# Optimization experiments

Measured on AMD Instinct MI355X. Metric: run time of the kernel, lower is better.

## Reference

```python
import jax, jax.numpy as jnp
import numpy as np
from jax import lax

DIM = 192
K = 3
K2 = K * K


def _conv1x1(x, W, b):
    # x: [B,C,H,W], W: [O,C], b: [O]
    return jnp.einsum('oc,bchw->bohw', W, x) + b[None, :, None, None]


def setup_inputs() -> dict:
    key = jax.random.key(0)
    ks = jax.random.split(key, 10)
    B, C, H, Wd = 16, DIM, 96, 96
    s = 1.0 / np.sqrt(C)
    x = jax.random.normal(ks[0], (B, C, H, Wd), dtype=jnp.float32)
    Wk = jax.random.uniform(ks[1], (C, C), jnp.float32, -s, s)
    bk = jax.random.uniform(ks[2], (C,), jnp.float32, -s, s)
    sg = 1.0 / np.sqrt(K2)
    Wg = jax.random.uniform(ks[3], (K2, K2), jnp.float32, -sg, sg)
    bg = jax.random.uniform(ks[4], (K2,), jnp.float32, -sg, sg)
    Wx = jax.random.uniform(ks[5], (C, C), jnp.float32, -s, s)
    bx = jax.random.uniform(ks[6], (C,), jnp.float32, -s, s)
    Wp = jax.random.uniform(ks[7], (C, C), jnp.float32, -s, s)
    bp = jax.random.uniform(ks[8], (C,), jnp.float32, -s, s)
    dc = jnp.zeros((C,), jnp.float32)  # difference_control init
    return {"x": x, "Wk": Wk, "bk": bk, "Wg": Wg, "bg": bg,
            "Wx": Wx, "bx": bx, "Wp": Wp, "bp": bp, "dc": dc}


def reference(x, Wk, bk, Wg, bg, Wx, bx, Wp, bp, dc):
    B, C, H, Wd = x.shape
    L = H * Wd
    # --- kernel generation ---
    k = _conv1x1(x, Wk, bk)                       # [B,C,H,W]
    k = k.reshape(B, C, K2, L // K2).mean(-1)     # AdaptiveAvgPool1d(9), L % 9 == 0
    k = jax.nn.gelu(k, approximate=False)         # torch nn.GELU (exact erf)
    k = k @ Wg.T + bg                             # Linear(9,9)
    k = k.reshape(B, C, K, K)
    # --- kernel mean difference ---
    mean_k = k.mean(axis=(2, 3), keepdims=True)
    factor = jax.nn.sigmoid(dc)[None, :, None, None]
    k = k - factor * mean_k
    # --- dynamic depthwise conv, groups = B*C ---
    xp = _conv1x1(x, Wx, bx)
    lhs = xp.reshape(1, B * C, H, Wd)
    rhs = k.reshape(B * C, 1, K, K)
    y = lax.conv_general_dilated(
        lhs, rhs, window_strides=(1, 1), padding='SAME',
        dimension_numbers=('NCHW', 'OIHW', 'NCHW'),
        feature_group_count=B * C)
    y = y.reshape(B, C, H, Wd)
    return _conv1x1(y, Wp, bp)
```

## Files before the change

kernel.cpp:

```cpp
#include <hip/hip_runtime.h>
#include <math.h>

#define CDIM 192
#define HWP 9216
#define WIMG 96
#define HIMG 96
#define BDIM 16

typedef float f32x4 __attribute__((ext_vector_type(4)));
typedef short bf16x8 __attribute__((ext_vector_type(8)));

__device__ __forceinline__ ushort f2bf(float f) {
    uint u = __builtin_bit_cast(uint, f);
    u += 0x7FFFu + ((u >> 16) & 1);
    return (ushort)(u >> 16);
}
__device__ __forceinline__ float bf2f(ushort h) {
    return __builtin_bit_cast(float, (uint)h << 16);
}

__global__ void prep_wfrag_kernel(const float* __restrict__ Wx, const float* __restrict__ Wp,
                                  ushort* __restrict__ WxF, ushort* __restrict__ WpF) {
    int t = blockIdx.x * 256 + threadIdx.x;
    int m = t / 4608;
    int r = t % 4608;
    int ks = r / 768, nf = (r / 64) % 12, l = r % 64;
    const float* W = m ? Wp : Wx;
    ushort* F = m ? WpF : WxF;
    int o = nf * 16 + (l & 15);
    int c0 = ks * 32 + (l >> 4) * 8;
    float4 a = *(const float4*)&W[o * CDIM + c0];
    float4 b = *(const float4*)&W[o * CDIM + c0 + 4];
    ushort* dst = F + (size_t)r * 8;
    dst[0] = f2bf(a.x); dst[1] = f2bf(a.y); dst[2] = f2bf(a.z); dst[3] = f2bf(a.w);
    dst[4] = f2bf(b.x); dst[5] = f2bf(b.y); dst[6] = f2bf(b.z); dst[7] = f2bf(b.w);
}

template<int IN_BF16, int OUT_BF16, int DO_POOL>
__global__ __launch_bounds__(256, 2) void convmfma_kernel(
    const void* __restrict__ in_, const ushort* __restrict__ Wf,
    const float* __restrict__ bias, void* __restrict__ out_,
    float* __restrict__ px) {
    const int p0 = blockIdx.x * 64;
    const int b = blockIdx.y;
    const int tid = threadIdx.x;
    const int l = tid & 63, w = tid >> 6;
    const size_t inplane = (size_t)CDIM * HWP;

    __shared__ __align__(16) ushort S[64 * 200];

#pragma unroll
    for (int it = 0; it < 3; ++it) {
        int u = tid + it * 256;
        int p4 = (u & 15) * 4, c4 = (u >> 4) * 4;
        ushort vv[4][4];
        if (IN_BF16) {
            const ushort* inb = (const ushort*)in_ + (size_t)b * inplane;
#pragma unroll
            for (int r = 0; r < 4; ++r) {
                ushort4 t4 = *(const ushort4*)(inb + (size_t)(c4 + r) * HWP + p0 + p4);
                vv[r][0] = t4.x; vv[r][1] = t4.y; vv[r][2] = t4.z; vv[r][3] = t4.w;
            }
        } else {
            const float* inb = (const float*)in_ + (size_t)b * inplane;
#pragma unroll
            for (int r = 0; r < 4; ++r) {
                float4 t4 = *(const float4*)(inb + (size_t)(c4 + r) * HWP + p0 + p4);
                vv[r][0] = f2bf(t4.x); vv[r][1] = f2bf(t4.y);
                vv[r][2] = f2bf(t4.z); vv[r][3] = f2bf(t4.w);
            }
        }
#pragma unroll
        for (int q = 0; q < 4; ++q) {
            *(ushort4*)&S[(p4 + q) * 200 + c4] =
                make_ushort4(vv[0][q], vv[1][q], vv[2][q], vv[3][q]);
        }
    }
    __syncthreads();

    if (DO_POOL) {
        if (tid < CDIM) {
            float s = 0.f;
#pragma unroll 8
            for (int p = 0; p < 64; ++p) s += bf2f(S[p * 200 + tid]);
            atomicAdd(&px[(b * CDIM + tid) * 9 + (p0 >> 10)], s);
        }
    }

    f32x4 acc[12];
#pragma unroll
    for (int nf = 0; nf < 12; ++nf) {
        float bv = bias[nf * 16 + (l & 15)];
        acc[nf] = (f32x4){bv, bv, bv, bv};
    }

    const ushort* Sp = &S[(w * 16 + (l & 15)) * 200];
    const int g8 = (l >> 4) * 8;
#pragma unroll
    for (int ks = 0; ks < 6; ++ks) {
        bf16x8 a = *(const bf16x8*)(Sp + ks * 32 + g8);
#pragma unroll
        for (int nf = 0; nf < 12; ++nf) {
            bf16x8 bb = *(const bf16x8*)&Wf[(size_t)((ks * 12 + nf) * 64 + l) * 8];
            acc[nf] = __builtin_amdgcn_mfma_f32_16x16x32_bf16(a, bb, acc[nf], 0, 0, 0);
        }
    }

    const int p_out = p0 + w * 16 + (l >> 4) * 4;
#pragma unroll
    for (int nf = 0; nf < 12; ++nf) {
        int o = nf * 16 + (l & 15);
        if (OUT_BF16) {
            ushort* ob = (ushort*)out_ + (size_t)b * inplane + (size_t)o * HWP + p_out;
            *(ushort4*)ob = make_ushort4(f2bf(acc[nf][0]), f2bf(acc[nf][1]),
                                         f2bf(acc[nf][2]), f2bf(acc[nf][3]));
        } else {
            float* ob = (float*)out_ + (size_t)b * inplane + (size_t)o * HWP + p_out;
            *(float4*)ob = make_float4(acc[nf][0], acc[nf][1], acc[nf][2], acc[nf][3]);
        }
    }
}

__global__ void make_kernels_kernel(const float* __restrict__ px,
                                    const float* __restrict__ Wk, const float* __restrict__ bk,
                                    const float* __restrict__ Wg, const float* __restrict__ bg,
                                    const float* __restrict__ dc,
                                    float* __restrict__ kk) {
    int b = blockIdx.x;
    int o = threadIdx.x;
    __shared__ float pxs[CDIM * 9];
    for (int i = threadIdx.x; i < CDIM * 9; i += blockDim.x)
        pxs[i] = px[b * CDIM * 9 + i] * (1.0f / 1024.0f);
    __syncthreads();
    float k1[9];
    float bias = bk[o];
#pragma unroll
    for (int j = 0; j < 9; j++) k1[j] = bias;
    for (int c = 0; c < CDIM; c++) {
        float w = Wk[o * CDIM + c];
#pragma unroll
        for (int j = 0; j < 9; j++) k1[j] = fmaf(w, pxs[c * 9 + j], k1[j]);
    }
#pragma unroll
    for (int j = 0; j < 9; j++) {
        float v = k1[j];
        k1[j] = 0.5f * v * (1.0f + erff(v * 0.70710678118654752f));
    }
    float k2[9];
    float mean = 0.f;
#pragma unroll
    for (int i = 0; i < 9; i++) {
        float a = bg[i];
#pragma unroll
        for (int j = 0; j < 9; j++) a = fmaf(k1[j], Wg[i * 9 + j], a);
        k2[i] = a;
        mean += a;
    }
    mean *= (1.0f / 9.0f);
    float f = 1.0f / (1.0f + expf(-dc[o]));
    float sub = f * mean;
#pragma unroll
    for (int i = 0; i < 9; i++) kk[(b * CDIM + o) * 9 + i] = k2[i] - sub;
}

#define SROW 100
template<int OUT_BF16>
__global__ __launch_bounds__(256) void dwconv_kernel_bf16(const ushort* __restrict__ xp,
                                                          const float* __restrict__ kk,
                                                          void* __restrict__ y_) {
    int bc = blockIdx.x >> 1;
    int row0 = (blockIdx.x & 1) * 48;
    int tid = threadIdx.x;

    __shared__ __align__(16) float Sbuf[4 + 50 * SROW + 4];
    float* S = Sbuf + 4;

    float kv[9];
#pragma unroll
    for (int j = 0; j < 9; j++) kv[j] = kk[bc * 9 + j];

    float4 z4 = make_float4(0.f, 0.f, 0.f, 0.f);
    for (int i = tid; i < (4 + 50 * SROW + 4) / 4; i += 256) ((float4*)Sbuf)[i] = z4;
    __syncthreads();

    const ushort* src = xp + (size_t)bc * HWP;
    for (int i = tid; i < 50 * 24; i += 256) {
        int s = i / 24, j4 = i % 24;
        int hh = row0 - 1 + s;
        if (hh >= 0 && hh < HIMG) {
            ushort4 v = *(const ushort4*)(src + (size_t)hh * WIMG + 4 * j4);
            *(float4*)&S[s * SROW + 4 * j4] =
                make_float4(bf2f(v.x), bf2f(v.y), bf2f(v.z), bf2f(v.w));
        }
    }
    __syncthreads();

    for (int i = tid; i < 48 * 24; i += 256) {
        int h = i / 24, wg = i % 24;
        float a0 = 0.f, a1 = 0.f, a2 = 0.f, a3 = 0.f;
#pragma unroll
        for (int r = 0; r < 3; r++) {
            const float* row = &S[(h + r) * SROW + 4 * wg];
            float left = row[-1];
            float4 m = *(const float4*)row;
            float r4 = row[4];
            float c0 = kv[r * 3 + 0], c1 = kv[r * 3 + 1], c2 = kv[r * 3 + 2];
            a0 = fmaf(c0, left, fmaf(c1, m.x, fmaf(c2, m.y, a0)));
            a1 = fmaf(c0, m.x, fmaf(c1, m.y, fmaf(c2, m.z, a1)));
            a2 = fmaf(c0, m.y, fmaf(c1, m.z, fmaf(c2, m.w, a2)));
            a3 = fmaf(c0, m.z, fmaf(c1, m.w, fmaf(c2, r4, a3)));
        }
        if (OUT_BF16) {
            ushort* dst = (ushort*)y_ + (size_t)bc * HWP;
            *(ushort4*)(dst + (size_t)(row0 + h) * WIMG + 4 * wg) =
                make_ushort4(f2bf(a0), f2bf(a1), f2bf(a2), f2bf(a3));
        } else {
            float* dst = (float*)y_ + (size_t)bc * HWP;
            *(float4*)(dst + (size_t)(row0 + h) * WIMG + 4 * wg) =
                make_float4(a0, a1, a2, a3);
        }
    }
}

extern "C" void kernel_launch(void* const* d_in, const int* in_sizes, int n_in,
                              void* d_out, int out_size, void* d_ws, size_t ws_size,
                              hipStream_t stream) {
    const float* x  = (const float*)d_in[0];
    const float* Wk = (const float*)d_in[1];
    const float* bk = (const float*)d_in[2];
    const float* Wg = (const float*)d_in[3];
    const float* bg = (const float*)d_in[4];
    const float* Wx = (const float*)d_in[5];
    const float* bx = (const float*)d_in[6];
    const float* Wp = (const float*)d_in[7];
    const float* bp = (const float*)d_in[8];
    const float* dc = (const float*)d_in[9];
    float* out = (float*)d_out;

    char* ws = (char*)d_ws;
    size_t off_WxF = 0;
    size_t off_WpF = off_WxF + 36864 * 2;
    size_t off_px  = off_WpF + 36864 * 2;
    size_t off_kk  = off_px + 27648 * 4;
    size_t off_xp  = off_kk + 27648 * 4;
    size_t xp_bytes = (size_t)BDIM * CDIM * HWP * 2;
    size_t off_y   = off_xp + xp_bytes;

    ushort* WxF = (ushort*)(ws + off_WxF);
    ushort* WpF = (ushort*)(ws + off_WpF);
    float*  px  = (float*)(ws + off_px);
    float*  kkp = (float*)(ws + off_kk);
    ushort* xp  = (ushort*)(ws + off_xp);
    bool y_in_ws = (ws_size >= off_y + xp_bytes);

    hipMemsetAsync(px, 0, 27648 * 4, stream);
    prep_wfrag_kernel<<<dim3(36), dim3(256), 0, stream>>>(Wx, Wp, WxF, WpF);
    convmfma_kernel<0, 1, 1><<<dim3(HWP / 64, BDIM), dim3(256), 0, stream>>>(
        (const void*)x, WxF, bx, (void*)xp, px);
    make_kernels_kernel<<<dim3(BDIM), dim3(CDIM), 0, stream>>>(px, Wk, bk, Wg, bg, dc, kkp);

    if (y_in_ws) {
        ushort* y = (ushort*)(ws + off_y);
        dwconv_kernel_bf16<1><<<dim3(BDIM * CDIM * 2), dim3(256), 0, stream>>>(xp, kkp, (void*)y);
        convmfma_kernel<1, 0, 0><<<dim3(HWP / 64, BDIM), dim3(256), 0, stream>>>(
            (const void*)y, WpF, bp, (void*)out, nullptr);
    } else {
        dwconv_kernel_bf16<0><<<dim3(BDIM * CDIM * 2), dim3(256), 0, stream>>>(xp, kkp, (void*)out);
        convmfma_kernel<0, 0, 0><<<dim3(HWP / 64, BDIM), dim3(256), 0, stream>>>(
            (const void*)out, WpF, bp, (void*)out, nullptr);
    }
}
```

Before: 341.4 us.

## Load MFMA A-operands directly from global, drop LDS staging, raise occupancy

The 1x1-conv MFMA kernel no longer stages the input tile through shared memory. Each lane now loads its A fragments straight from global memory with scalar strided loads, and the pooling sum is done with wave shuffles plus atomics instead of an LDS column sum. Launch bounds go from 2 to 3 blocks per SM, and the make_kernels kernel now stages Wk through padded shared memory to avoid uncoalesced per-thread row reads. The direct loads are scalar 2- or 4-byte accesses strided by a full plane, which risks poorer coalescing, more memory instructions, and more atomics than the previous vectorized LDS transpose.

```diff
diff --git a/kernel.cpp b/kernel.cpp
--- a/kernel.cpp
+++ b/kernel.cpp
@@ -37,7 +37,7 @@
 }
 
 template<int IN_BF16, int OUT_BF16, int DO_POOL>
-__global__ __launch_bounds__(256, 2) void convmfma_kernel(
+__global__ __launch_bounds__(256, 3) void convmfma_kernel(
     const void* __restrict__ in_, const ushort* __restrict__ Wf,
     const float* __restrict__ bias, void* __restrict__ out_,
     float* __restrict__ px) {
@@ -45,46 +45,45 @@
     const int b = blockIdx.y;
     const int tid = threadIdx.x;
     const int l = tid & 63, w = tid >> 6;
-    const size_t inplane = (size_t)CDIM * HWP;
-
-    __shared__ __align__(16) ushort S[64 * 200];
-
-#pragma unroll
-    for (int it = 0; it < 3; ++it) {
-        int u = tid + it * 256;
-        int p4 = (u & 15) * 4, c4 = (u >> 4) * 4;
-        ushort vv[4][4];
-        if (IN_BF16) {
-            const ushort* inb = (const ushort*)in_ + (size_t)b * inplane;
-#pragma unroll
-            for (int r = 0; r < 4; ++r) {
-                ushort4 t4 = *(const ushort4*)(inb + (size_t)(c4 + r) * HWP + p0 + p4);
-                vv[r][0] = t4.x; vv[r][1] = t4.y; vv[r][2] = t4.z; vv[r][3] = t4.w;
-            }
-        } else {
-            const float* inb = (const float*)in_ + (size_t)b * inplane;
-#pragma unroll
-            for (int r = 0; r < 4; ++r) {
-                float4 t4 = *(const float4*)(inb + (size_t)(c4 + r) * HWP + p0 + p4);
-                vv[r][0] = f2bf(t4.x); vv[r][1] = f2bf(t4.y);
-                vv[r][2] = f2bf(t4.z); vv[r][3] = f2bf(t4.w);
-            }
-        }
-#pragma unroll
-        for (int q = 0; q < 4; ++q) {
-            *(ushort4*)&S[(p4 + q) * 200 + c4] =
-                make_ushort4(vv[0][q], vv[1][q], vv[2][q], vv[3][q]);
-        }
-    }
-    __syncthreads();
-
-    if (DO_POOL) {
-        if (tid < CDIM) {
-            float s = 0.f;
-#pragma unroll 8
-            for (int p = 0; p < 64; ++p) s += bf2f(S[p * 200 + tid]);
-            atomicAdd(&px[(b * CDIM + tid) * 9 + (p0 >> 10)], s);
-        }
+    const size_t plane = (size_t)CDIM * HWP;
+    const int pA = p0 + w * 16 + (l & 15);
+    const int g8 = (l >> 4) * 8;
+
+    bf16x8 a[6];
+    if (IN_BF16) {
+        const ushort* inb = (const ushort*)in_ + (size_t)b * plane + pA;
+#pragma unroll
+        for (int ks = 0; ks < 6; ++ks) {
+#pragma unroll
+            for (int i = 0; i < 8; ++i)
+                a[ks][i] = (short)inb[(size_t)(ks * 32 + g8 + i) * HWP];
+        }
+    } else {
+        const float* inb = (const float*)in_ + (size_t)b * plane + pA;
+        float af[6][8];
+#pragma unroll
+        for (int ks = 0; ks < 6; ++ks)
+#pragma unroll
+            for (int i = 0; i < 8; ++i)
+                af[ks][i] = inb[(size_t)(ks * 32 + g8 + i) * HWP];
+        if (DO_POOL) {
+#pragma unroll
+            for (int ks = 0; ks < 6; ++ks)
+#pragma unroll
+                for (int i = 0; i < 8; ++i) {
+                    float s = af[ks][i];
+                    s += __shfl_xor(s, 1, 64);
+                    s += __shfl_xor(s, 2, 64);
+                    s += __shfl_xor(s, 4, 64);
+                    s += __shfl_xor(s, 8, 64);
+                    if ((l & 15) == 0)
+                        atomicAdd(&px[(b * CDIM + ks * 32 + g8 + i) * 9 + (p0 >> 10)], s);
+                }
+        }
+#pragma unroll
+        for (int ks = 0; ks < 6; ++ks)
+#pragma unroll
+            for (int i = 0; i < 8; ++i) a[ks][i] = (short)f2bf(af[ks][i]);
     }
 
     f32x4 acc[12];
@@ -94,15 +93,12 @@
         acc[nf] = (f32x4){bv, bv, bv, bv};
     }
 
-    const ushort* Sp = &S[(w * 16 + (l & 15)) * 200];
-    const int g8 = (l >> 4) * 8;
 #pragma unroll
     for (int ks = 0; ks < 6; ++ks) {
-        bf16x8 a = *(const bf16x8*)(Sp + ks * 32 + g8);
 #pragma unroll
         for (int nf = 0; nf < 12; ++nf) {
             bf16x8 bb = *(const bf16x8*)&Wf[(size_t)((ks * 12 + nf) * 64 + l) * 8];
-            acc[nf] = __builtin_amdgcn_mfma_f32_16x16x32_bf16(a, bb, acc[nf], 0, 0, 0);
+            acc[nf] = __builtin_amdgcn_mfma_f32_16x16x32_bf16(a[ks], bb, acc[nf], 0, 0, 0);
         }
     }
 
@@ -111,11 +107,11 @@
     for (int nf = 0; nf < 12; ++nf) {
         int o = nf * 16 + (l & 15);
         if (OUT_BF16) {
-            ushort* ob = (ushort*)out_ + (size_t)b * inplane + (size_t)o * HWP + p_out;
+            ushort* ob = (ushort*)out_ + (size_t)b * plane + (size_t)o * HWP + p_out;
             *(ushort4*)ob = make_ushort4(f2bf(acc[nf][0]), f2bf(acc[nf][1]),
                                          f2bf(acc[nf][2]), f2bf(acc[nf][3]));
         } else {
-            float* ob = (float*)out_ + (size_t)b * inplane + (size_t)o * HWP + p_out;
+            float* ob = (float*)out_ + (size_t)b * plane + (size_t)o * HWP + p_out;
             *(float4*)ob = make_float4(acc[nf][0], acc[nf][1], acc[nf][2], acc[nf][3]);
         }
     }
@@ -129,17 +125,27 @@
     int b = blockIdx.x;
     int o = threadIdx.x;
     __shared__ float pxs[CDIM * 9];
-    for (int i = threadIdx.x; i < CDIM * 9; i += blockDim.x)
+    __shared__ float WkS[CDIM][33];
+    for (int i = threadIdx.x; i < CDIM * 9; i += CDIM)
         pxs[i] = px[b * CDIM * 9 + i] * (1.0f / 1024.0f);
-    __syncthreads();
     float k1[9];
     float bias = bk[o];
 #pragma unroll
     for (int j = 0; j < 9; j++) k1[j] = bias;
-    for (int c = 0; c < CDIM; c++) {
-        float w = Wk[o * CDIM + c];
-#pragma unroll
-        for (int j = 0; j < 9; j++) k1[j] = fmaf(w, pxs[c * 9 + j], k1[j]);
+
+    for (int c0 = 0; c0 < CDIM; c0 += 32) {
+        __syncthreads();
+        for (int i = threadIdx.x; i < CDIM * 32; i += CDIM) {
+            int oo = i >> 5, cc = i & 31;
+            WkS[oo][cc] = Wk[oo * CDIM + c0 + cc];
+        }
+        __syncthreads();
+#pragma unroll 4
+        for (int cc = 0; cc < 32; ++cc) {
+            float wv = WkS[o][cc];
+#pragma unroll
+            for (int j = 0; j < 9; j++) k1[j] = fmaf(wv, pxs[(c0 + cc) * 9 + j], k1[j]);
+        }
     }
 #pragma unroll
     for (int j = 0; j < 9; j++) {
```

Result: slower. 450.4 us (+31.9%).

## Switch intermediates to channels-last layout with swizzled LDS and direct MFMA loads

Applied to the files above, without the earlier changes.

The xp and y intermediates are now stored in channels-last (pixel-major) bf16 layout. The first 1x1 conv transposes its output through XOR-swizzled LDS so the writes are coalesced. The second 1x1 conv loads its A fragments straight from global memory with no LDS staging. The depthwise conv becomes one thread per 8 channels per pixel, reading neighbours as 16-byte vectors with transposed kernel weights, and make_kernels now tiles Wk through LDS. This removes the LDS transpose in conv2 and the separate plane staging in dwconv, at the cost of the dwconv reading neighbours from global or cache nine times.

```diff
diff --git a/kernel.cpp b/kernel.cpp
--- a/kernel.cpp
+++ b/kernel.cpp
@@ -17,6 +17,10 @@
 }
 __device__ __forceinline__ float bf2f(ushort h) {
     return __builtin_bit_cast(float, (uint)h << 16);
+}
+
+__device__ __forceinline__ int sidx(int p, int c) {
+    return (p << 8) + (c ^ ((((p >> 2) ^ p) & 7) << 3));
 }
 
 __global__ void prep_wfrag_kernel(const float* __restrict__ Wx, const float* __restrict__ Wp,
@@ -36,55 +40,41 @@
     dst[4] = f2bf(b.x); dst[5] = f2bf(b.y); dst[6] = f2bf(b.z); dst[7] = f2bf(b.w);
 }
 
-template<int IN_BF16, int OUT_BF16, int DO_POOL>
-__global__ __launch_bounds__(256, 2) void convmfma_kernel(
-    const void* __restrict__ in_, const ushort* __restrict__ Wf,
-    const float* __restrict__ bias, void* __restrict__ out_,
+__global__ __launch_bounds__(256, 2) void conv1_kernel(
+    const float* __restrict__ x, const ushort* __restrict__ Wf,
+    const float* __restrict__ bias, ushort* __restrict__ xp,
     float* __restrict__ px) {
     const int p0 = blockIdx.x * 64;
     const int b = blockIdx.y;
     const int tid = threadIdx.x;
     const int l = tid & 63, w = tid >> 6;
-    const size_t inplane = (size_t)CDIM * HWP;
-
-    __shared__ __align__(16) ushort S[64 * 200];
-
+
+    __shared__ __align__(16) ushort S[64 * 256];
+
+    const float* inb = x + (size_t)b * CDIM * HWP;
 #pragma unroll
     for (int it = 0; it < 3; ++it) {
         int u = tid + it * 256;
         int p4 = (u & 15) * 4, c4 = (u >> 4) * 4;
         ushort vv[4][4];
-        if (IN_BF16) {
-            const ushort* inb = (const ushort*)in_ + (size_t)b * inplane;
-#pragma unroll
-            for (int r = 0; r < 4; ++r) {
-                ushort4 t4 = *(const ushort4*)(inb + (size_t)(c4 + r) * HWP + p0 + p4);
-                vv[r][0] = t4.x; vv[r][1] = t4.y; vv[r][2] = t4.z; vv[r][3] = t4.w;
-            }
-        } else {
-            const float* inb = (const float*)in_ + (size_t)b * inplane;
-#pragma unroll
-            for (int r = 0; r < 4; ++r) {
-                float4 t4 = *(const float4*)(inb + (size_t)(c4 + r) * HWP + p0 + p4);
-                vv[r][0] = f2bf(t4.x); vv[r][1] = f2bf(t4.y);
-                vv[r][2] = f2bf(t4.z); vv[r][3] = f2bf(t4.w);
-            }
-        }
-#pragma unroll
-        for (int q = 0; q < 4; ++q) {
-            *(ushort4*)&S[(p4 + q) * 200 + c4] =
+#pragma unroll
+        for (int r = 0; r < 4; ++r) {
+            float4 t4 = *(const float4*)(inb + (size_t)(c4 + r) * HWP + p0 + p4);
+            vv[r][0] = f2bf(t4.x); vv[r][1] = f2bf(t4.y);
+            vv[r][2] = f2bf(t4.z); vv[r][3] = f2bf(t4.w);
+        }
+#pragma unroll
+        for (int q = 0; q < 4; ++q)
+            *(ushort4*)&S[sidx(p4 + q, c4)] =
                 make_ushort4(vv[0][q], vv[1][q], vv[2][q], vv[3][q]);
-        }
     }
     __syncthreads();
 
-    if (DO_POOL) {
-        if (tid < CDIM) {
-            float s = 0.f;
+    if (tid < CDIM) {
+        float s = 0.f;
 #pragma unroll 8
-            for (int p = 0; p < 64; ++p) s += bf2f(S[p * 200 + tid]);
-            atomicAdd(&px[(b * CDIM + tid) * 9 + (p0 >> 10)], s);
-        }
+        for (int p = 0; p < 64; ++p) s += bf2f(S[sidx(p, tid)]);
+        atomicAdd(&px[(b * CDIM + tid) * 9 + (p0 >> 10)], s);
     }
 
     f32x4 acc[12];
@@ -94,30 +84,73 @@
         acc[nf] = (f32x4){bv, bv, bv, bv};
     }
 
-    const ushort* Sp = &S[(w * 16 + (l & 15)) * 200];
     const int g8 = (l >> 4) * 8;
+    const int prow = w * 16 + (l & 15);
 #pragma unroll
     for (int ks = 0; ks < 6; ++ks) {
-        bf16x8 a = *(const bf16x8*)(Sp + ks * 32 + g8);
+        bf16x8 a = *(const bf16x8*)&S[sidx(prow, ks * 32 + g8)];
 #pragma unroll
         for (int nf = 0; nf < 12; ++nf) {
             bf16x8 bb = *(const bf16x8*)&Wf[(size_t)((ks * 12 + nf) * 64 + l) * 8];
             acc[nf] = __builtin_amdgcn_mfma_f32_16x16x32_bf16(a, bb, acc[nf], 0, 0, 0);
         }
     }
+    __syncthreads();
+
+    const int pw = w * 16 + (l >> 4) * 4;
+#pragma unroll
+    for (int nf = 0; nf < 12; ++nf) {
+        int o = nf * 16 + (l & 15);
+#pragma unroll
+        for (int q = 0; q < 4; ++q) S[sidx(pw + q, o)] = f2bf(acc[nf][q]);
+    }
+    __syncthreads();
+
+    ushort* ob = xp + ((size_t)b * HWP + p0) * CDIM;
+#pragma unroll
+    for (int it = 0; it < 6; ++it) {
+        int u = tid + it * 256;
+        int r = u / 24, cg = u % 24;
+        *(bf16x8*)(ob + (size_t)r * CDIM + cg * 8) = *(const bf16x8*)&S[sidx(r, cg * 8)];
+    }
+}
+
+__global__ __launch_bounds__(256, 3) void conv2_kernel(
+    const ushort* __restrict__ y, const ushort* __restrict__ Wf,
+    const float* __restrict__ bias, float* __restrict__ out) {
+    const int p0 = blockIdx.x * 64;
+    const int b = blockIdx.y;
+    const int l = threadIdx.x & 63, w = threadIdx.x >> 6;
+    const int g8 = (l >> 4) * 8;
+    const int pA = p0 + w * 16 + (l & 15);
+
+    const ushort* yb = y + ((size_t)b * HWP + pA) * CDIM + g8;
+    bf16x8 a[6];
+#pragma unroll
+    for (int ks = 0; ks < 6; ++ks) a[ks] = *(const bf16x8*)(yb + ks * 32);
+
+    f32x4 acc[12];
+#pragma unroll
+    for (int nf = 0; nf < 12; ++nf) {
+        float bv = bias[nf * 16 + (l & 15)];
+        acc[nf] = (f32x4){bv, bv, bv, bv};
+    }
+#pragma unroll
+    for (int ks = 0; ks < 6; ++ks) {
+#pragma unroll
+        for (int nf = 0; nf < 12; ++nf) {
+            bf16x8 bb = *(const bf16x8*)&Wf[(size_t)((ks * 12 + nf) * 64 + l) * 8];
+            acc[nf] = __builtin_amdgcn_mfma_f32_16x16x32_bf16(a[ks], bb, acc[nf], 0, 0, 0);
+        }
+    }
 
     const int p_out = p0 + w * 16 + (l >> 4) * 4;
+    float* ob = out + (size_t)b * CDIM * HWP + p_out;
 #pragma unroll
     for (int nf = 0; nf < 12; ++nf) {
         int o = nf * 16 + (l & 15);
-        if (OUT_BF16) {
-            ushort* ob = (ushort*)out_ + (size_t)b * inplane + (size_t)o * HWP + p_out;
-            *(ushort4*)ob = make_ushort4(f2bf(acc[nf][0]), f2bf(acc[nf][1]),
-                                         f2bf(acc[nf][2]), f2bf(acc[nf][3]));
-        } else {
-            float* ob = (float*)out_ + (size_t)b * inplane + (size_t)o * HWP + p_out;
-            *(float4*)ob = make_float4(acc[nf][0], acc[nf][1], acc[nf][2], acc[nf][3]);
-        }
+        *(float4*)(ob + (size_t)o * HWP) =
+            make_float4(acc[nf][0], acc[nf][1], acc[nf][2], acc[nf][3]);
     }
 }
 
@@ -125,21 +158,31 @@
                                     const float* __restrict__ Wk, const float* __restrict__ bk,
                                     const float* __restrict__ Wg, const float* __restrict__ bg,
                                     const float* __restrict__ dc,
-                                    float* __restrict__ kk) {
+                                    float* __restrict__ kkT) {
     int b = blockIdx.x;
     int o = threadIdx.x;
     __shared__ float pxs[CDIM * 9];
-    for (int i = threadIdx.x; i < CDIM * 9; i += blockDim.x)
+    __shared__ float WkS[CDIM][33];
+    for (int i = threadIdx.x; i < CDIM * 9; i += CDIM)
         pxs[i] = px[b * CDIM * 9 + i] * (1.0f / 1024.0f);
-    __syncthreads();
     float k1[9];
     float bias = bk[o];
 #pragma unroll
     for (int j = 0; j < 9; j++) k1[j] = bias;
-    for (int c = 0; c < CDIM; c++) {
-        float w = Wk[o * CDIM + c];
-#pragma unroll
-        for (int j = 0; j < 9; j++) k1[j] = fmaf(w, pxs[c * 9 + j], k1[j]);
+
+    for (int c0 = 0; c0 < CDIM; c0 += 32) {
+        __syncthreads();
+        for (int i = threadIdx.x; i < CDIM * 32; i += CDIM) {
+            int oo = i >> 5, cc = i & 31;
+            WkS[oo][cc] = Wk[oo * CDIM + c0 + cc];
+        }
+        __syncthreads();
+#pragma unroll 4
+        for (int cc = 0; cc < 32; ++cc) {
+            float wv = WkS[o][cc];
+#pragma unroll
+            for (int j = 0; j < 9; j++) k1[j] = fmaf(wv, pxs[(c0 + cc) * 9 + j], k1[j]);
+        }
     }
 #pragma unroll
     for (int j = 0; j < 9; j++) {
@@ -160,66 +203,52 @@
     float f = 1.0f / (1.0f + expf(-dc[o]));
     float sub = f * mean;
 #pragma unroll
-    for (int i = 0; i < 9; i++) kk[(b * CDIM + o) * 9 + i] = k2[i] - sub;
-}
-
-#define SROW 100
-template<int OUT_BF16>
-__global__ __launch_bounds__(256) void dwconv_kernel_bf16(const ushort* __restrict__ xp,
-                                                          const float* __restrict__ kk,
-                                                          void* __restrict__ y_) {
-    int bc = blockIdx.x >> 1;
-    int row0 = (blockIdx.x & 1) * 48;
-    int tid = threadIdx.x;
-
-    __shared__ __align__(16) float Sbuf[4 + 50 * SROW + 4];
-    float* S = Sbuf + 4;
-
-    float kv[9];
-#pragma unroll
-    for (int j = 0; j < 9; j++) kv[j] = kk[bc * 9 + j];
-
-    float4 z4 = make_float4(0.f, 0.f, 0.f, 0.f);
-    for (int i = tid; i < (4 + 50 * SROW + 4) / 4; i += 256) ((float4*)Sbuf)[i] = z4;
-    __syncthreads();
-
-    const ushort* src = xp + (size_t)bc * HWP;
-    for (int i = tid; i < 50 * 24; i += 256) {
-        int s = i / 24, j4 = i % 24;
-        int hh = row0 - 1 + s;
-        if (hh >= 0 && hh < HIMG) {
-            ushort4 v = *(const ushort4*)(src + (size_t)hh * WIMG + 4 * j4);
-            *(float4*)&S[s * SROW + 4 * j4] =
-                make_float4(bf2f(v.x), bf2f(v.y), bf2f(v.z), bf2f(v.w));
-        }
-    }
-    __syncthreads();
-
-    for (int i = tid; i < 48 * 24; i += 256) {
-        int h = i / 24, wg = i % 24;
-        float a0 = 0.f, a1 = 0.f, a2 = 0.f, a3 = 0.f;
-#pragma unroll
-        for (int r = 0; r < 3; r++) {
-            const float* row = &S[(h + r) * SROW + 4 * wg];
-            float left = row[-1];
-            float4 m = *(const float4*)row;
-            float r4 = row[4];
-            float c0 = kv[r * 3 + 0], c1 = kv[r * 3 + 1], c2 = kv[r * 3 + 2];
-            a0 = fmaf(c0, left, fmaf(c1, m.x, fmaf(c2, m.y, a0)));
-            a1 = fmaf(c0, m.x, fmaf(c1, m.y, fmaf(c2, m.z, a1)));
-            a2 = fmaf(c0, m.y, fmaf(c1, m.z, fmaf(c2, m.w, a2)));
-            a3 = fmaf(c0, m.z, fmaf(c1, m.w, fmaf(c2, r4, a3)));
-        }
-        if (OUT_BF16) {
-            ushort* dst = (ushort*)y_ + (size_t)bc * HWP;
-            *(ushort4*)(dst + (size_t)(row0 + h) * WIMG + 4 * wg) =
-                make_ushort4(f2bf(a0), f2bf(a1), f2bf(a2), f2bf(a3));
-        } else {
-            float* dst = (float*)y_ + (size_t)bc * HWP;
-            *(float4*)(dst + (size_t)(row0 + h) * WIMG + 4 * wg) =
-                make_float4(a0, a1, a2, a3);
-        }
-    }
+    for (int i = 0; i < 9; i++) kkT[(b * 9 + i) * CDIM + o] = k2[i] - sub;
+}
+
+__global__ __launch_bounds__(256) void dwconv_cl_kernel(const ushort* __restrict__ xp,
+                                                        const float* __restrict__ kkT,
+                                                        ushort* __restrict__ y) {
+    int idx = blockIdx.x * 256 + threadIdx.x;
+    int cg = idx % 24;
+    int pb = idx / 24;
+    int p = pb % HWP, b = pb / HWP;
+    int h = p / WIMG, wq = p % WIMG;
+
+    const ushort* base = xp + (size_t)pb * CDIM + cg * 8;
+    const float* kb = kkT + (size_t)b * 9 * CDIM + cg * 8;
+
+    float acc[8];
+#pragma unroll
+    for (int i = 0; i < 8; ++i) acc[i] = 0.f;
+
+#pragma unroll
+    for (int dh = -1; dh <= 1; ++dh) {
+        int hh = h + dh;
+        if (hh < 0 || hh >= HIMG) continue;
+#pragma unroll
+        for (int dw = -1; dw <= 1; ++dw) {
+            int ww = wq + dw;
+            if (ww < 0 || ww >= WIMG) continue;
+            int j = (dh + 1) * 3 + (dw + 1);
+            bf16x8 v = *(const bf16x8*)(base + (ptrdiff_t)(dh * WIMG + dw) * CDIM);
+            float4 k0 = *(const float4*)(kb + j * CDIM);
+            float4 k1 = *(const float4*)(kb + j * CDIM + 4);
+            acc[0] = fmaf(bf2f((ushort)v[0]), k0.x, acc[0]);
+            acc[1] = fmaf(bf2f((ushort)v[1]), k0.y, acc[1]);
+            acc[2] = fmaf(bf2f((ushort)v[2]), k0.z, acc[2]);
+            acc[3] = fmaf(bf2f((ushort)v[3]), k0.w, acc[3]);
+            acc[4] = fmaf(bf2f((ushort)v[4]), k1.x, acc[4]);
+            acc[5] = fmaf(bf2f((ushort)v[5]), k1.y, acc[5]);
+            acc[6] = fmaf(bf2f((ushort)v[6]), k1.z, acc[6]);
+            acc[7] = fmaf(bf2f((ushort)v[7]), k1.w, acc[7]);
+        }
+    }
+    ushort* dst = y + (size_t)pb * CDIM + cg * 8;
+    ushort4 o0 = make_ushort4(f2bf(acc[0]), f2bf(acc[1]), f2bf(acc[2]), f2bf(acc[3]));
+    ushort4 o1 = make_ushort4(f2bf(acc[4]), f2bf(acc[5]), f2bf(acc[6]), f2bf(acc[7]));
+    *(ushort4*)dst = o0;
+    *(ushort4*)(dst + 4) = o1;
 }
 
 extern "C" void kernel_launch(void* const* d_in, const int* in_sizes, int n_in,
@@ -249,24 +278,14 @@
     ushort* WxF = (ushort*)(ws + off_WxF);
     ushort* WpF = (ushort*)(ws + off_WpF);
     float*  px  = (float*)(ws + off_px);
-    float*  kkp = (float*)(ws + off_kk);
+    float*  kkT = (float*)(ws + off_kk);
     ushort* xp  = (ushort*)(ws + off_xp);
-    bool y_in_ws = (ws_size >= off_y + xp_bytes);
+    ushort* y   = (ushort*)(ws + off_y);
 
     hipMemsetAsync(px, 0, 27648 * 4, stream);
     prep_wfrag_kernel<<<dim3(36), dim3(256), 0, stream>>>(Wx, Wp, WxF, WpF);
-    convmfma_kernel<0, 1, 1><<<dim3(HWP / 64, BDIM), dim3(256), 0, stream>>>(
-        (const void*)x, WxF, bx, (void*)xp, px);
-    make_kernels_kernel<<<dim3(BDIM), dim3(CDIM), 0, stream>>>(px, Wk, bk, Wg, bg, dc, kkp);
-
-    if (y_in_ws) {
-        ushort* y = (ushort*)(ws + off_y);
-        dwconv_kernel_bf16<1><<<dim3(BDIM * CDIM * 2), dim3(256), 0, stream>>>(xp, kkp, (void*)y);
-        convmfma_kernel<1, 0, 0><<<dim3(HWP / 64, BDIM), dim3(256), 0, stream>>>(
-            (const void*)y, WpF, bp, (void*)out, nullptr);
-    } else {
-        dwconv_kernel_bf16<0><<<dim3(BDIM * CDIM * 2), dim3(256), 0, stream>>>(xp, kkp, (void*)out);
-        convmfma_kernel<0, 0, 0><<<dim3(HWP / 64, BDIM), dim3(256), 0, stream>>>(
-            (const void*)out, WpF, bp, (void*)out, nullptr);
-    }
-}
+    conv1_kernel<<<dim3(HWP / 64, BDIM), dim3(256), 0, stream>>>(x, WxF, bx, xp, px);
+    make_kernels_kernel<<<dim3(BDIM), dim3(CDIM), 0, stream>>>(px, Wk, bk, Wg, bg, dc, kkT);
+    dwconv_cl_kernel<<<dim3((size_t)BDIM * HWP * 24 / 256), dim3(256), 0, stream>>>(xp, kkT, y);
+    conv2_kernel<<<dim3(HWP / 64, BDIM), dim3(256), 0, stream>>>(y, WpF, bp, out);
+}
```

Result: slower. 351.3 us (+2.9%).
